# Optimization experiments

Measured on AMD Instinct MI355X. Metric: run time of the kernel, lower is better.

Reference implementation:

```python
import jax, jax.numpy as jnp
import numpy as np

ALPHA = 0.2  # LeakyReLU negative slope
NEG_INF = -9e15


def setup_inputs() -> dict:
    key = jax.random.key(0)
    k1, k2, k3, k4 = jax.random.split(key, 4)
    N, F_IN, F_OUT = 8192, 128, 64
    h = jax.random.normal(k1, (N, F_IN), dtype=jnp.float32)
    adj = jax.random.randint(k2, (N, N), 0, 2, dtype=jnp.int32)
    # xavier_uniform with gain=1.414 (as in the torch module)
    gain = 1.414
    bW = gain * np.sqrt(6.0 / (F_IN + F_OUT))
    W = jax.random.uniform(k3, (F_IN, F_OUT), dtype=jnp.float32, minval=-bW, maxval=bW)
    ba = gain * np.sqrt(6.0 / (2 * F_OUT + 1))
    a = jax.random.uniform(k4, (2 * F_OUT, 1), dtype=jnp.float32, minval=-ba, maxval=ba)
    return {"h": h, "adj": adj, "W": W, "a": a}


def reference(h, adj, W, a):
    # Wh: [N, F_out]
    Wh = h @ W
    F_out = Wh.shape[1]
    # Decompose a^T [Wh_i || Wh_j] = (Wh @ a_src)_i + (Wh @ a_dst)_j
    # (same math as the repeat+concat construction, without the N*N*2F tensor)
    src = Wh @ a[:F_out, 0]   # [N]
    dst = Wh @ a[F_out:, 0]   # [N]
    e = jax.nn.leaky_relu(src[:, None] + dst[None, :], negative_slope=ALPHA)  # [N, N]
    e = jnp.where(adj > 0, e, jnp.float32(NEG_INF))
    attention = jax.nn.softmax(e, axis=1)  # [N, N]
    h_prime = attention @ Wh               # [N, F_out]
    return jax.nn.elu(h_prime)
```

## Files before the change

kernel.cpp:

```cpp
#include <hip/hip_runtime.h>

#define ALPHA 0.2f
#define NN 8192
#define FIN 128
#define FOUT 64

typedef short bf16x8 __attribute__((ext_vector_type(8)));
typedef float f32x4 __attribute__((ext_vector_type(4)));

__global__ __launch_bounds__(256) void gat_k0(const int* __restrict__ adj,
                                              unsigned long long* __restrict__ adjb) {
    int t = threadIdx.x, w = t >> 6, l = t & 63;
    int row = blockIdx.x * 4 + w;
    const int4* a4 = (const int4*)(adj + (size_t)row * NN);
    unsigned long long* ob = adjb + (size_t)row * 32 * 4;
#pragma unroll 4
    for (int it = 0; it < 32; ++it) {
        int4 av = a4[it * 64 + l];
        unsigned long long b0 = __ballot(av.x != 0);
        unsigned long long b1 = __ballot(av.y != 0);
        unsigned long long b2 = __ballot(av.z != 0);
        unsigned long long b3 = __ballot(av.w != 0);
        if (l == 0) {
            ulonglong4 v;
            v.x = b0; v.y = b1; v.z = b2; v.w = b3;
            *(ulonglong4*)(ob + it * 4) = v;
        }
    }
}

__global__ __launch_bounds__(256) void gat_k1(const float* __restrict__ h,
                                              const float* __restrict__ W,
                                              const float* __restrict__ a,
                                              float* __restrict__ Wh,
                                              float* __restrict__ src,
                                              float* __restrict__ dst) {
    __shared__ float wlds[FIN * FOUT];
    int t = threadIdx.x;
    const float4* W4 = (const float4*)W;
    float4* wlds4 = (float4*)wlds;
#pragma unroll
    for (int q = 0; q < 8; ++q) wlds4[q * 256 + t] = W4[q * 256 + t];
    __syncthreads();
    int wave = t >> 6, lane = t & 63;
    int row = blockIdx.x * 4 + wave;
    const float4* h4 = (const float4*)(h + (size_t)row * FIN);
    float acc = 0.f;
#pragma unroll
    for (int k4 = 0; k4 < 32; ++k4) {
        float4 hv = h4[k4];
        acc = fmaf(hv.x, wlds[(k4 * 4 + 0) * 64 + lane], acc);
        acc = fmaf(hv.y, wlds[(k4 * 4 + 1) * 64 + lane], acc);
        acc = fmaf(hv.z, wlds[(k4 * 4 + 2) * 64 + lane], acc);
        acc = fmaf(hv.w, wlds[(k4 * 4 + 3) * 64 + lane], acc);
    }
    Wh[(size_t)row * 64 + lane] = acc;
    float sa = acc * a[lane];
    float da = acc * a[64 + lane];
#pragma unroll
    for (int off = 32; off; off >>= 1) {
        sa += __shfl_xor(sa, off);
        da += __shfl_xor(da, off);
    }
    if (lane == 0) { src[row] = sa; dst[row] = da; }
}

__global__ __launch_bounds__(256) void gat_k1b(const float* __restrict__ Wh,
                                               uint4* __restrict__ whbt2) {
    __shared__ float wt[32 * 64];
    int tid = threadIdx.x;
    int t = blockIdx.x;
    const float4* s4 = (const float4*)(Wh + (size_t)t * 2048);
    float4* l4 = (float4*)wt;
    l4[tid] = s4[tid];
    l4[tid + 256] = s4[tid + 256];
    __syncthreads();
    int q = tid >> 6, l = tid & 63, r = l & 15, g = l >> 4;
    unsigned pk[4];
#pragma unroll
    for (int k = 0; k < 4; ++k) {
        float lo = wt[(8 * g + 2 * k + 0) * 64 + 16 * q + r];
        float hi = wt[(8 * g + 2 * k + 1) * 64 + 16 * q + r];
        asm("v_cvt_pk_bf16_f32 %0, %1, %2" : "=v"(pk[k]) : "v"(lo), "v"(hi));
    }
    whbt2[(size_t)t * 256 + tid] = make_uint4(pk[0], pk[1], pk[2], pk[3]);
}

__global__ __launch_bounds__(256, 4) void gat_k2(const unsigned long long* __restrict__ adjb,
                                                 const uint4* __restrict__ whbt2,
                                                 const float* __restrict__ src,
                                                 const float* __restrict__ dst,
                                                 float* __restrict__ pl,
                                                 float* __restrict__ pacc,
                                                 int ns, int js) {
    const int l = threadIdx.x & 63;
    const int w = threadIdx.x >> 6;
    const int r = l & 15;
    const int g = l >> 4;
    const int s = blockIdx.x;
    const int rg = blockIdx.y;
    const int task = rg * ns + s;
    const int row = rg * 64 + w * 16 + r;
    const int j0 = s * js;
    const int steps = js >> 5;

    const float srcv = src[row];
    const float4* dst4 = (const float4*)dst;
    const ulonglong2* brow2 = (const ulonglong2*)(adjb + (size_t)row * 128);
    const uint4* bt = whbt2 + l;

    f32x4 acc0 = {0.f, 0.f, 0.f, 0.f}, acc1 = acc0, acc2 = acc0, acc3 = acc0, accl = acc0;
    bf16x8 bones;
#pragma unroll
    for (int e = 0; e < 8; ++e) bones[e] = (short)0x3F80;

    int jh = j0;
    uint4 b0 = bt[(jh >> 5) * 256 + 0 * 64];
    uint4 b1 = bt[(jh >> 5) * 256 + 1 * 64];
    uint4 b2 = bt[(jh >> 5) * 256 + 2 * 64];
    uint4 b3 = bt[(jh >> 5) * 256 + 3 * 64];
    ulonglong2 mA = brow2[(jh >> 8) * 2 + 0];
    ulonglong2 mB = brow2[(jh >> 8) * 2 + 1];

    for (int t = 0; t < steps; ++t, jh += 32) {
        const int jn = (t + 1 < steps) ? jh + 32 : j0;
        uint4 nb0 = bt[(jn >> 5) * 256 + 0 * 64];
        uint4 nb1 = bt[(jn >> 5) * 256 + 1 * 64];
        uint4 nb2 = bt[(jn >> 5) * 256 + 2 * 64];
        uint4 nb3 = bt[(jn >> 5) * 256 + 3 * 64];
        ulonglong2 nmA = brow2[(jn >> 8) * 2 + 0];
        ulonglong2 nmB = brow2[(jn >> 8) * 2 + 1];

        float4 d0 = dst4[(jh >> 2) + 2 * g];
        float4 d1 = dst4[(jh >> 2) + 2 * g + 1];
        const int hb = ((jh >> 5) & 7) * 8 + 2 * g;
        const unsigned long long m0 = mA.x, m1 = mA.y, m2 = mB.x, m3 = mB.y;

        float p[8];
        {
            float xs[8] = {d0.x, d0.y, d0.z, d0.w, d1.x, d1.y, d1.z, d1.w};
#pragma unroll
            for (int e = 0; e < 8; ++e) {
                float x = srcv + xs[e];
                float lr = fmaxf(x, 0.f) + ALPHA * fminf(x, 0.f);
                float pe = __expf(lr);
                unsigned long long mm = (e & 3) == 0 ? m0 : (e & 3) == 1 ? m1
                                      : (e & 3) == 2 ? m2 : m3;
                unsigned bit = (unsigned)(mm >> (hb + (e >> 2))) & 1u;
                p[e] = bit ? pe : 0.f;
            }
        }
        unsigned pw0, pw1, pw2, pw3;
        asm("v_cvt_pk_bf16_f32 %0, %1, %2" : "=v"(pw0) : "v"(p[0]), "v"(p[1]));
        asm("v_cvt_pk_bf16_f32 %0, %1, %2" : "=v"(pw1) : "v"(p[2]), "v"(p[3]));
        asm("v_cvt_pk_bf16_f32 %0, %1, %2" : "=v"(pw2) : "v"(p[4]), "v"(p[5]));
        asm("v_cvt_pk_bf16_f32 %0, %1, %2" : "=v"(pw3) : "v"(p[6]), "v"(p[7]));
        bf16x8 af = __builtin_bit_cast(bf16x8, make_uint4(pw0, pw1, pw2, pw3));

        acc0 = __builtin_amdgcn_mfma_f32_16x16x32_bf16(af, __builtin_bit_cast(bf16x8, b0), acc0, 0, 0, 0);
        acc1 = __builtin_amdgcn_mfma_f32_16x16x32_bf16(af, __builtin_bit_cast(bf16x8, b1), acc1, 0, 0, 0);
        acc2 = __builtin_amdgcn_mfma_f32_16x16x32_bf16(af, __builtin_bit_cast(bf16x8, b2), acc2, 0, 0, 0);
        acc3 = __builtin_amdgcn_mfma_f32_16x16x32_bf16(af, __builtin_bit_cast(bf16x8, b3), acc3, 0, 0, 0);
        accl = __builtin_amdgcn_mfma_f32_16x16x32_bf16(af, bones, accl, 0, 0, 0);

        b0 = nb0; b1 = nb1; b2 = nb2; b3 = nb3;
        mA = nmA; mB = nmB;
    }

    if (r == 0) {
        float* plo = pl + (size_t)task * 64 + w * 16 + g * 4;
        plo[0] = accl[0]; plo[1] = accl[1]; plo[2] = accl[2]; plo[3] = accl[3];
    }

    float* po = pacc + (size_t)task * 4096 + (size_t)(w * 16) * 64;
#pragma unroll
    for (int reg = 0; reg < 4; ++reg) {
        int m = g * 4 + reg;
        po[m * 64 + 0 * 16 + r] = acc0[reg];
        po[m * 64 + 1 * 16 + r] = acc1[reg];
        po[m * 64 + 2 * 16 + r] = acc2[reg];
        po[m * 64 + 3 * 16 + r] = acc3[reg];
    }
}

__global__ __launch_bounds__(256) void gat_k3(const float* __restrict__ pl,
                                              const float* __restrict__ pacc,
                                              float* __restrict__ out, int ns) {
    int t = threadIdx.x;
    int wave = t >> 6, lane = t & 63;
    int row = blockIdx.x * 4 + wave;
    int rg = row >> 6, rr = row & 63;
    float L = 0.f, o = 0.f;
    for (int s2 = 0; s2 < ns; ++s2) {
        L += pl[(size_t)(rg * ns + s2) * 64 + rr];
        o += pacc[(size_t)(rg * ns + s2) * 4096 + rr * 64 + lane];
    }
    float hp = o / L;
    out[(size_t)row * 64 + lane] = hp > 0.f ? hp : __expf(hp) - 1.f;
}

extern "C" void kernel_launch(void* const* d_in, const int* in_sizes, int n_in,
                              void* d_out, int out_size, void* d_ws, size_t ws_size,
                              hipStream_t stream) {
    const float* h = (const float*)d_in[0];
    const int* adj = (const int*)d_in[1];
    const float* W = (const float*)d_in[2];
    const float* a = (const float*)d_in[3];
    float* out = (float*)d_out;
    float* ws = (float*)d_ws;

    size_t avail = ws_size / sizeof(float);
    int ns = 8;
    while (ns > 1 && (size_t)2899968 + (size_t)ns * 532480 > avail) ns >>= 1;
    int js = NN / ns;

    float* Wh = ws;
    float* src = Wh + (size_t)NN * FOUT;
    float* dst = src + NN;
    float* pl = dst + NN;
    float* pacc = pl + (size_t)128 * ns * 64;
    uint4* whbt2 = (uint4*)(pacc + (size_t)128 * ns * 4096);
    unsigned long long* adjb = (unsigned long long*)((float*)whbt2 + 262144);

    gat_k0<<<dim3(NN / 4), dim3(256), 0, stream>>>(adj, adjb);
    gat_k1<<<dim3(NN / 4), dim3(256), 0, stream>>>(h, W, a, Wh, src, dst);
    gat_k1b<<<dim3(NN / 32), dim3(256), 0, stream>>>(Wh, whbt2);
    gat_k2<<<dim3(ns, 128), dim3(256), 0, stream>>>(adjb, whbt2, src, dst, pl, pacc, ns, js);
    gat_k3<<<dim3(NN / 4), dim3(256), 0, stream>>>(pl, pacc, out, ns);
}
```

Before: 445.9 us.

## Stage Wh tiles, mask bits and dst in LDS with fixed 16-way j split

The attention-aggregation kernel now copies its 512-column slice of bf16 Wh, the adjacency bitmask words and the dst scores into shared memory once per block, then runs a fully unrolled 16-step MFMA loop that reads operands from LDS instead of global memory. The j-split is fixed at 16 chunks (up from a workspace-dependent 8), doubling the grid and the partial-sum traffic into the reduction kernel. Occupancy hint drops to 2 blocks per CU because of the roughly 70KB LDS footprint. The workspace-size check is removed, so a too-small workspace is no longer handled, and an unused f2b helper is added.

Measured after the change: 420.0 us. -5.8%, faster.

```diff
diff --git a/kernel.cpp b/kernel.cpp
--- a/kernel.cpp
+++ b/kernel.cpp
@@ -4,9 +4,17 @@
 #define NN 8192
 #define FIN 128
 #define FOUT 64
+#define NS 16
+#define JS 512
 
 typedef short bf16x8 __attribute__((ext_vector_type(8)));
 typedef float f32x4 __attribute__((ext_vector_type(4)));
+
+__device__ __forceinline__ unsigned short f2b(float x) {
+    unsigned u = __builtin_bit_cast(unsigned, x);
+    unsigned r = (u + 0x7fffu + ((u >> 16) & 1u)) >> 16;
+    return (unsigned short)r;
+}
 
 __global__ __launch_bounds__(256) void gat_k0(const int* __restrict__ adj,
                                               unsigned long long* __restrict__ adjb) {
@@ -86,59 +94,68 @@
     whbt2[(size_t)t * 256 + tid] = make_uint4(pk[0], pk[1], pk[2], pk[3]);
 }
 
-__global__ __launch_bounds__(256, 4) void gat_k2(const unsigned long long* __restrict__ adjb,
+__global__ __launch_bounds__(256, 2) void gat_k2(const unsigned long long* __restrict__ adjb,
                                                  const uint4* __restrict__ whbt2,
                                                  const float* __restrict__ src,
                                                  const float* __restrict__ dst,
                                                  float* __restrict__ pl,
-                                                 float* __restrict__ pacc,
-                                                 int ns, int js) {
-    const int l = threadIdx.x & 63;
-    const int w = threadIdx.x >> 6;
-    const int r = l & 15;
-    const int g = l >> 4;
-    const int s = blockIdx.x;
-    const int rg = blockIdx.y;
-    const int task = rg * ns + s;
-    const int row = rg * 64 + w * 16 + r;
-    const int j0 = s * js;
-    const int steps = js >> 5;
+                                                 float* __restrict__ pacc) {
+    __shared__ uint4 lds_b[16 * 256];
+    __shared__ ulonglong2 lds_m[4 * 64];
+    __shared__ float lds_d[JS];
+    const int tid = threadIdx.x;
+    const int l = tid & 63, w = tid >> 6;
+    const int r = l & 15, g = l >> 4;
+    const int s = blockIdx.x, rg = blockIdx.y;
+    const int task = rg * NS + s;
+    const int rowbase = rg * 64;
+    const int rho = w * 16 + r;
+    const int row = rowbase + rho;
+    const int j0 = s * JS;
+
+    const uint4* bsrc = whbt2 + (size_t)(j0 >> 5) * 256;
+#pragma unroll
+    for (int k = 0; k < 16; ++k) lds_b[k * 256 + tid] = bsrc[k * 256 + tid];
+    {
+        const ulonglong2* msrc =
+            (const ulonglong2*)(adjb + (size_t)(rowbase + (tid & 63)) * 128 + (size_t)(j0 >> 8) * 4) + (tid >> 6);
+        lds_m[tid] = *msrc;
+    }
+    if (tid < JS / 4) ((float4*)lds_d)[tid] = ((const float4*)(dst + j0))[tid];
+    __syncthreads();
 
     const float srcv = src[row];
-    const float4* dst4 = (const float4*)dst;
-    const ulonglong2* brow2 = (const ulonglong2*)(adjb + (size_t)row * 128);
-    const uint4* bt = whbt2 + l;
-
     f32x4 acc0 = {0.f, 0.f, 0.f, 0.f}, acc1 = acc0, acc2 = acc0, acc3 = acc0, accl = acc0;
     bf16x8 bones;
 #pragma unroll
     for (int e = 0; e < 8; ++e) bones[e] = (short)0x3F80;
 
-    int jh = j0;
-    uint4 b0 = bt[(jh >> 5) * 256 + 0 * 64];
-    uint4 b1 = bt[(jh >> 5) * 256 + 1 * 64];
-    uint4 b2 = bt[(jh >> 5) * 256 + 2 * 64];
-    uint4 b3 = bt[(jh >> 5) * 256 + 3 * 64];
-    ulonglong2 mA = brow2[(jh >> 8) * 2 + 0];
-    ulonglong2 mB = brow2[(jh >> 8) * 2 + 1];
-
-    for (int t = 0; t < steps; ++t, jh += 32) {
-        const int jn = (t + 1 < steps) ? jh + 32 : j0;
-        uint4 nb0 = bt[(jn >> 5) * 256 + 0 * 64];
-        uint4 nb1 = bt[(jn >> 5) * 256 + 1 * 64];
-        uint4 nb2 = bt[(jn >> 5) * 256 + 2 * 64];
-        uint4 nb3 = bt[(jn >> 5) * 256 + 3 * 64];
-        ulonglong2 nmA = brow2[(jn >> 8) * 2 + 0];
-        ulonglong2 nmB = brow2[(jn >> 8) * 2 + 1];
-
-        float4 d0 = dst4[(jh >> 2) + 2 * g];
-        float4 d1 = dst4[(jh >> 2) + 2 * g + 1];
-        const int hb = ((jh >> 5) & 7) * 8 + 2 * g;
-        const unsigned long long m0 = mA.x, m1 = mA.y, m2 = mB.x, m3 = mB.y;
+    ulonglong2 g0a = lds_m[0 * 64 + rho], g0b = lds_m[1 * 64 + rho];
+    ulonglong2 g1a = lds_m[2 * 64 + rho], g1b = lds_m[3 * 64 + rho];
+
+    uint4 cb0 = lds_b[0 * 64 + l], cb1 = lds_b[1 * 64 + l], cb2 = lds_b[2 * 64 + l], cb3 = lds_b[3 * 64 + l];
+    float4 cd0 = *(const float4*)(lds_d + g * 8);
+    float4 cd1 = *(const float4*)(lds_d + g * 8 + 4);
+
+#pragma unroll
+    for (int t = 0; t < 16; ++t) {
+        const int tn = (t + 1) & 15;
+        uint4 nb0 = lds_b[tn * 256 + 0 * 64 + l];
+        uint4 nb1 = lds_b[tn * 256 + 1 * 64 + l];
+        uint4 nb2 = lds_b[tn * 256 + 2 * 64 + l];
+        uint4 nb3 = lds_b[tn * 256 + 3 * 64 + l];
+        float4 nd0 = *(const float4*)(lds_d + tn * 32 + g * 8);
+        float4 nd1 = *(const float4*)(lds_d + tn * 32 + g * 8 + 4);
+
+        const unsigned long long m0 = (t < 8) ? g0a.x : g1a.x;
+        const unsigned long long m1 = (t < 8) ? g0a.y : g1a.y;
+        const unsigned long long m2 = (t < 8) ? g0b.x : g1b.x;
+        const unsigned long long m3 = (t < 8) ? g0b.y : g1b.y;
+        const int hb = (t & 7) * 8 + 2 * g;
 
         float p[8];
         {
-            float xs[8] = {d0.x, d0.y, d0.z, d0.w, d1.x, d1.y, d1.z, d1.w};
+            float xs[8] = {cd0.x, cd0.y, cd0.z, cd0.w, cd1.x, cd1.y, cd1.z, cd1.w};
 #pragma unroll
             for (int e = 0; e < 8; ++e) {
                 float x = srcv + xs[e];
@@ -157,14 +174,14 @@
         asm("v_cvt_pk_bf16_f32 %0, %1, %2" : "=v"(pw3) : "v"(p[6]), "v"(p[7]));
         bf16x8 af = __builtin_bit_cast(bf16x8, make_uint4(pw0, pw1, pw2, pw3));
 
-        acc0 = __builtin_amdgcn_mfma_f32_16x16x32_bf16(af, __builtin_bit_cast(bf16x8, b0), acc0, 0, 0, 0);
-        acc1 = __builtin_amdgcn_mfma_f32_16x16x32_bf16(af, __builtin_bit_cast(bf16x8, b1), acc1, 0, 0, 0);
-        acc2 = __builtin_amdgcn_mfma_f32_16x16x32_bf16(af, __builtin_bit_cast(bf16x8, b2), acc2, 0, 0, 0);
-        acc3 = __builtin_amdgcn_mfma_f32_16x16x32_bf16(af, __builtin_bit_cast(bf16x8, b3), acc3, 0, 0, 0);
+        acc0 = __builtin_amdgcn_mfma_f32_16x16x32_bf16(af, __builtin_bit_cast(bf16x8, cb0), acc0, 0, 0, 0);
+        acc1 = __builtin_amdgcn_mfma_f32_16x16x32_bf16(af, __builtin_bit_cast(bf16x8, cb1), acc1, 0, 0, 0);
+        acc2 = __builtin_amdgcn_mfma_f32_16x16x32_bf16(af, __builtin_bit_cast(bf16x8, cb2), acc2, 0, 0, 0);
+        acc3 = __builtin_amdgcn_mfma_f32_16x16x32_bf16(af, __builtin_bit_cast(bf16x8, cb3), acc3, 0, 0, 0);
         accl = __builtin_amdgcn_mfma_f32_16x16x32_bf16(af, bones, accl, 0, 0, 0);
 
-        b0 = nb0; b1 = nb1; b2 = nb2; b3 = nb3;
-        mA = nmA; mB = nmB;
+        cb0 = nb0; cb1 = nb1; cb2 = nb2; cb3 = nb3;
+        cd0 = nd0; cd1 = nd1;
     }
 
     if (r == 0) {
@@ -185,15 +202,15 @@
 
 __global__ __launch_bounds__(256) void gat_k3(const float* __restrict__ pl,
                                               const float* __restrict__ pacc,
-                                              float* __restrict__ out, int ns) {
+                                              float* __restrict__ out) {
     int t = threadIdx.x;
     int wave = t >> 6, lane = t & 63;
     int row = blockIdx.x * 4 + wave;
     int rg = row >> 6, rr = row & 63;
     float L = 0.f, o = 0.f;
-    for (int s2 = 0; s2 < ns; ++s2) {
-        L += pl[(size_t)(rg * ns + s2) * 64 + rr];
-        o += pacc[(size_t)(rg * ns + s2) * 4096 + rr * 64 + lane];
+    for (int s2 = 0; s2 < NS; ++s2) {
+        L += pl[(size_t)(rg * NS + s2) * 64 + rr];
+        o += pacc[(size_t)(rg * NS + s2) * 4096 + rr * 64 + lane];
     }
     float hp = o / L;
     out[(size_t)row * 64 + lane] = hp > 0.f ? hp : __expf(hp) - 1.f;
@@ -209,22 +226,17 @@
     float* out = (float*)d_out;
     float* ws = (float*)d_ws;
 
-    size_t avail = ws_size / sizeof(float);
-    int ns = 8;
-    while (ns > 1 && (size_t)2899968 + (size_t)ns * 532480 > avail) ns >>= 1;
-    int js = NN / ns;
-
     float* Wh = ws;
     float* src = Wh + (size_t)NN * FOUT;
     float* dst = src + NN;
     float* pl = dst + NN;
-    float* pacc = pl + (size_t)128 * ns * 64;
-    uint4* whbt2 = (uint4*)(pacc + (size_t)128 * ns * 4096);
+    float* pacc = pl + (size_t)128 * NS * 64;
+    uint4* whbt2 = (uint4*)(pacc + (size_t)128 * NS * 4096);
     unsigned long long* adjb = (unsigned long long*)((float*)whbt2 + 262144);
 
     gat_k0<<<dim3(NN / 4), dim3(256), 0, stream>>>(adj, adjb);
     gat_k1<<<dim3(NN / 4), dim3(256), 0, stream>>>(h, W, a, Wh, src, dst);
     gat_k1b<<<dim3(NN / 32), dim3(256), 0, stream>>>(Wh, whbt2);
-    gat_k2<<<dim3(ns, 128), dim3(256), 0, stream>>>(adjb, whbt2, src, dst, pl, pacc, ns, js);
-    gat_k3<<<dim3(NN / 4), dim3(256), 0, stream>>>(pl, pacc, out, ns);
-}
+    gat_k2<<<dim3(NS, 128), dim3(256), 0, stream>>>(adjb, whbt2, src, dst, pl, pacc);
+    gat_k3<<<dim3(NN / 4), dim3(256), 0, stream>>>(pl, pacc, out);
+}
```
